# Kernel optimization log

Hardware: AMD Instinct MI355X
Metric: run time of the kernel (lower is better)

The kernel has to match this reference:

```python
import jax, jax.numpy as jnp
import numpy as np

D_MODEL = 1024
HEAD_DIM = D_MODEL // 16  # num_heads=16, used only for the softmax scale
EPS = 1e-5


def _layernorm(x, g, b):
    mu = jnp.mean(x, axis=-1, keepdims=True)
    var = jnp.var(x, axis=-1, keepdims=True)
    return (x - mu) * jax.lax.rsqrt(var + EPS) * g + b


def setup_inputs() -> dict:
    key = jax.random.key(0)
    ks = jax.random.split(key, 16)
    d, dff = D_MODEL, 4 * D_MODEL
    s = 1.0 / np.sqrt(d)
    inp = {
        "x": jax.random.normal(ks[0], (4, 2048, d), dtype=jnp.float32),
        "wq": jax.random.normal(ks[1], (d, d), dtype=jnp.float32) * s,
        "bq": jnp.zeros((d,), jnp.float32),
        "wk": jax.random.normal(ks[2], (d, d), dtype=jnp.float32) * s,
        "bk": jnp.zeros((d,), jnp.float32),
        "wv": jax.random.normal(ks[3], (d, d), dtype=jnp.float32) * s,
        "bv": jnp.zeros((d,), jnp.float32),
        "wo": jax.random.normal(ks[4], (d, d), dtype=jnp.float32) * s,
        "bo": jnp.zeros((d,), jnp.float32),
        "w1": jax.random.normal(ks[5], (d, dff), dtype=jnp.float32) * s,
        "b1": jnp.zeros((dff,), jnp.float32),
        "w2": jax.random.normal(ks[6], (dff, d), dtype=jnp.float32) * (1.0 / np.sqrt(dff)),
        "b2": jnp.zeros((d,), jnp.float32),
        "g1": jnp.ones((d,), jnp.float32),
        "be1": jnp.zeros((d,), jnp.float32),
        "g2": jnp.ones((d,), jnp.float32),
        "be2": jnp.zeros((d,), jnp.float32),
    }
    return inp


def reference(x, wq, bq, wk, bk, wv, bv, wo, bo, w1, b1, w2, b2, g1, be1, g2, be2):
    # --- attention sub-block (NOTE: no head split in original module) ---
    residual = x
    h = _layernorm(x, g1, be1)
    q = h @ wq + bq
    k = h @ wk + bk
    v = h @ wv + bv
    scale = 1.0 / np.sqrt(HEAD_DIM)
    scores = jnp.einsum("bsd,btd->bst", q, k) * scale  # [B,S,S]
    attn = jax.nn.softmax(scores, axis=-1)
    ctx = jnp.einsum("bst,btd->bsd", attn, v)
    x = ctx @ wo + bo + residual
    # --- MLP sub-block ---
    residual = x
    h = _layernorm(x, g2, be2)
    h = jax.nn.gelu(h @ w1 + b1, approximate=False)
    return h @ w2 + b2 + residual
```

## Files before the change

kernel.cpp:

```cpp
#include <hip/hip_runtime.h>
#include <hip/hip_bf16.h>

typedef __hip_bfloat16 bf16;
typedef __attribute__((ext_vector_type(8))) short short8;
typedef __attribute__((ext_vector_type(4))) float floatx4;

__device__ __forceinline__ unsigned short f2bf(float x) {
  unsigned u = __builtin_bit_cast(unsigned, x);
  unsigned r = (u + 0x7fffu + ((u >> 16) & 1u)) >> 16;
  return (unsigned short)r;
}

#define GLL(g, l) __builtin_amdgcn_global_load_lds(                                  \
    (const __attribute__((address_space(1))) void*)(g),                              \
    (__attribute__((address_space(3))) void*)(l), 16, 0, 0)

template <int N> __device__ __forceinline__ void vmwait() {
  asm volatile("s_waitcnt vmcnt(%0)" ::"i"(N) : "memory");
}

__global__ __launch_bounds__(256) void wtrans_kernel(const float* __restrict__ in,
                                                     bf16* __restrict__ out,
                                                     int K, int N) {
  __shared__ float tile[32][33];
  int tx = threadIdx.x, ty = threadIdx.y;
  int n0 = blockIdx.x * 32, k0 = blockIdx.y * 32;
#pragma unroll
  for (int i = 0; i < 32; i += 8)
    tile[ty + i][tx] = in[(size_t)(k0 + ty + i) * N + (n0 + tx)];
  __syncthreads();
#pragma unroll
  for (int i = 0; i < 32; i += 8)
    out[(size_t)(n0 + ty + i) * K + (k0 + tx)] = __float2bfloat16(tile[tx][ty + i]);
}

__global__ __launch_bounds__(256) void ln_kernel(const float* __restrict__ x,
                                                 const float* __restrict__ g,
                                                 const float* __restrict__ b,
                                                 bf16* __restrict__ out) {
  const int D = 1024;
  size_t row = blockIdx.x;
  int t = threadIdx.x;
  float4 v = ((const float4*)(x + row * D))[t];
  float s  = v.x + v.y + v.z + v.w;
  float ss = v.x * v.x + v.y * v.y + v.z * v.z + v.w * v.w;
#pragma unroll
  for (int off = 32; off > 0; off >>= 1) {
    s  += __shfl_xor(s, off);
    ss += __shfl_xor(ss, off);
  }
  __shared__ float rs[4], rss[4];
  int wv = t >> 6;
  if ((t & 63) == 0) { rs[wv] = s; rss[wv] = ss; }
  __syncthreads();
  s  = rs[0] + rs[1] + rs[2] + rs[3];
  ss = rss[0] + rss[1] + rss[2] + rss[3];
  float mu  = s * (1.f / D);
  float inv = rsqrtf(ss * (1.f / D) - mu * mu + 1e-5f);
  float4 gv = ((const float4*)g)[t];
  float4 bv = ((const float4*)b)[t];
  ushort4 o;
  o.x = f2bf((v.x - mu) * inv * gv.x + bv.x);
  o.y = f2bf((v.y - mu) * inv * gv.y + bv.y);
  o.z = f2bf((v.z - mu) * inv * gv.z + bv.z);
  o.w = f2bf((v.w - mu) * inv * gv.w + bv.w);
  ((ushort4*)(out + row * D))[t] = o;
}

__global__ __launch_bounds__(256) void softmax_kernel(float* sc) {
  const int S = 2048;
  float* p = sc + (size_t)blockIdx.x * S;
  int t = threadIdx.x;
  float4 v0 = ((const float4*)p)[2 * t];
  float4 v1 = ((const float4*)p)[2 * t + 1];
  float f[8] = {v0.x, v0.y, v0.z, v0.w, v1.x, v1.y, v1.z, v1.w};
  float m = f[0];
#pragma unroll
  for (int j = 1; j < 8; ++j) m = fmaxf(m, f[j]);
#pragma unroll
  for (int off = 32; off > 0; off >>= 1) m = fmaxf(m, __shfl_xor(m, off));
  __shared__ float r1[4], r2[4];
  int wv = t >> 6;
  if ((t & 63) == 0) r1[wv] = m;
  __syncthreads();
  m = fmaxf(fmaxf(r1[0], r1[1]), fmaxf(r1[2], r1[3]));
  float s = 0.f;
#pragma unroll
  for (int j = 0; j < 8; ++j) { f[j] = __expf(f[j] - m); s += f[j]; }
#pragma unroll
  for (int off = 32; off > 0; off >>= 1) s += __shfl_xor(s, off);
  if ((t & 63) == 0) r2[wv] = s;
  __syncthreads();
  s = r2[0] + r2[1] + r2[2] + r2[3];
  float inv = 1.f / s;
  unsigned u0 = f2bf(f[0] * inv), u1 = f2bf(f[1] * inv);
  unsigned u2 = f2bf(f[2] * inv), u3 = f2bf(f[3] * inv);
  unsigned u4 = f2bf(f[4] * inv), u5 = f2bf(f[5] * inv);
  unsigned u6 = f2bf(f[6] * inv), u7 = f2bf(f[7] * inv);
  uint4 o;
  o.x = u0 | (u1 << 16);
  o.y = u2 | (u3 << 16);
  o.z = u4 | (u5 << 16);
  o.w = u6 | (u7 << 16);
  ((uint4*)p)[t] = o;
}

template <int NF, bool OUT_BF16, bool HAS_BIAS, bool HAS_RES, bool GELU, bool VTR>
__global__ __launch_bounds__(512, 2) void gemm4q(
    const bf16* __restrict__ A, int lda, size_t sA,
    const bf16* __restrict__ BT, int ldb, size_t sB,
    void* Cv, size_t sC,
    const float* __restrict__ bias, const float* res, bf16* vtr,
    int N, int K, float alpha, int gx, int gy) {
  constexpr int BN = NF * 64;
  constexpr int NI = NF / 2;
  constexpr int BHALF = NF == 4 ? 16384 : 8192;
  constexpr int W_A = 4;
  constexpr int W_B = NF == 4 ? 4 : 3;
  __shared__ __align__(16) char lds[65536 + (NF == 4 ? 65536 : 32768)];
  char* const ldsA = lds;
  char* const ldsB = lds + 65536;

  const int tid = threadIdx.x;
  const int lane = tid & 63;
  const int wave = tid >> 6;
  const int wm = wave >> 2, wn = wave & 3;
  const int lr = lane & 15, lq = lane >> 4;

  int id = blockIdx.x;
  const int nwg = gridDim.x;
  if ((nwg & 7) == 0) id = (id & 7) * (nwg >> 3) + (id >> 3);
  const int bx = id % gx;
  const int rem = id / gx;
  const int by = rem % gy;
  const int bz = rem / gy;
  const int m0 = by * 256, n0 = bx * BN;

  const int srow = tid >> 3;
  const int schunk = ((tid & 7) ^ (srow & 7)) * 8;
  const bf16* gA = A + sA * bz + (size_t)(m0 + srow) * lda + schunk;
  const bf16* gB = BT + sB * bz + (size_t)(n0 + srow) * ldb + schunk;

  const int nk = K >> 6;

  auto stA = [&](int tt, int h) {
    if (tt < nk) {
      const bf16* s = gA + (size_t)(h * 128) * lda + (size_t)tt * 64;
      char* d = ldsA + (((tt & 1) * 2 + h) << 14) + tid * 16;
      GLL(s, d);
      GLL(s + (size_t)64 * lda, d + 8192);
    }
  };
  auto stB = [&](int tt, int h) {
    if (tt < nk) {
      const bf16* s = gB + (size_t)(h * (BN / 2)) * ldb + (size_t)tt * 64;
      char* d = ldsB + ((tt & 1) * 2 + h) * BHALF + tid * 16;
      GLL(s, d);
      if constexpr (NF == 4) GLL(s + (size_t)64 * ldb, d + 8192);
    }
  };

  const int aB0 = (wm * 64 + lr) * 128 + ((lq ^ (lr & 7)) << 4);
  const int aB1 = aB0 ^ 64;
  const int bRow = (NF == 4) ? (wn * 32 + lr) : (wn * 16 + lr);
  const int bB0 = bRow * 128 + ((lq ^ (lr & 7)) << 4);
  const int bB1 = bB0 ^ 64;

  floatx4 acc[2][2][4][NI] = {};

  stA(0, 0); stB(0, 0); stB(0, 1); stA(0, 1);
  vmwait<W_B>();
  __builtin_amdgcn_s_barrier();

  for (int t = 0; t < nk; ++t) {
    const char* As0 = ldsA + (((t & 1) * 2 + 0) << 14);
    const char* As1 = ldsA + (((t & 1) * 2 + 1) << 14);
    const char* Bs0 = ldsB + ((t & 1) * 2 + 0) * BHALF;
    const char* Bs1 = ldsB + ((t & 1) * 2 + 1) * BHALF;
    short8 a0[4], a1[4], b0[NI], b1[NI];

#pragma unroll
    for (int mi = 0; mi < 4; ++mi) {
      a0[mi] = *(const short8*)(As0 + aB0 + mi * 2048);
      a1[mi] = *(const short8*)(As0 + aB1 + mi * 2048);
    }
#pragma unroll
    for (int ni = 0; ni < NI; ++ni) {
      b0[ni] = *(const short8*)(Bs0 + bB0 + ni * 2048);
      b1[ni] = *(const short8*)(Bs0 + bB1 + ni * 2048);
    }
    stA(t + 1, 0);
    asm volatile("s_waitcnt lgkmcnt(0)" ::: "memory");
    __builtin_amdgcn_sched_barrier(0);
    __builtin_amdgcn_s_setprio(1);
#pragma unroll
    for (int mi = 0; mi < 4; ++mi)
#pragma unroll
      for (int ni = 0; ni < NI; ++ni)
        acc[0][0][mi][ni] = __builtin_amdgcn_mfma_f32_16x16x32_bf16(a0[mi], b0[ni], acc[0][0][mi][ni], 0, 0, 0);
#pragma unroll
    for (int mi = 0; mi < 4; ++mi)
#pragma unroll
      for (int ni = 0; ni < NI; ++ni)
        acc[0][0][mi][ni] = __builtin_amdgcn_mfma_f32_16x16x32_bf16(a1[mi], b1[ni], acc[0][0][mi][ni], 0, 0, 0);
    __builtin_amdgcn_s_setprio(0);
    vmwait<W_A>();
    __builtin_amdgcn_s_barrier();

#pragma unroll
    for (int ni = 0; ni < NI; ++ni) {
      b0[ni] = *(const short8*)(Bs1 + bB0 + ni * 2048);
      b1[ni] = *(const short8*)(Bs1 + bB1 + ni * 2048);
    }
    stB(t + 1, 0);
    asm volatile("s_waitcnt lgkmcnt(0)" ::: "memory");
    __builtin_amdgcn_sched_barrier(0);
    __builtin_amdgcn_s_setprio(1);
#pragma unroll
    for (int mi = 0; mi < 4; ++mi)
#pragma unroll
      for (int ni = 0; ni < NI; ++ni)
        acc[0][1][mi][ni] = __builtin_amdgcn_mfma_f32_16x16x32_bf16(a0[mi], b0[ni], acc[0][1][mi][ni], 0, 0, 0);
#pragma unroll
    for (int mi = 0; mi < 4; ++mi)
#pragma unroll
      for (int ni = 0; ni < NI; ++ni)
        acc[0][1][mi][ni] = __builtin_amdgcn_mfma_f32_16x16x32_bf16(a1[mi], b1[ni], acc[0][1][mi][ni], 0, 0, 0);
    __builtin_amdgcn_s_setprio(0);
    vmwait<W_B>();
    __builtin_amdgcn_s_barrier();

#pragma unroll
    for (int mi = 0; mi < 4; ++mi) {
      a0[mi] = *(const short8*)(As1 + aB0 + mi * 2048);
      a1[mi] = *(const short8*)(As1 + aB1 + mi * 2048);
    }
    stB(t + 1, 1);
    asm volatile("s_waitcnt lgkmcnt(0)" ::: "memory");
    __builtin_amdgcn_sched_barrier(0);
    __builtin_amdgcn_s_setprio(1);
#pragma unroll
    for (int mi = 0; mi < 4; ++mi)
#pragma unroll
      for (int ni = 0; ni < NI; ++ni)
        acc[1][1][mi][ni] = __builtin_amdgcn_mfma_f32_16x16x32_bf16(a0[mi], b0[ni], acc[1][1][mi][ni], 0, 0, 0);
#pragma unroll
    for (int mi = 0; mi < 4; ++mi)
#pragma unroll
      for (int ni = 0; ni < NI; ++ni)
        acc[1][1][mi][ni] = __builtin_amdgcn_mfma_f32_16x16x32_bf16(a1[mi], b1[ni], acc[1][1][mi][ni], 0, 0, 0);
    __builtin_amdgcn_s_setprio(0);
    __builtin_amdgcn_s_barrier();

#pragma unroll
    for (int ni = 0; ni < NI; ++ni) {
      b0[ni] = *(const short8*)(Bs0 + bB0 + ni * 2048);
      b1[ni] = *(const short8*)(Bs0 + bB1 + ni * 2048);
    }
    stA(t + 1, 1);
    asm volatile("s_waitcnt lgkmcnt(0)" ::: "memory");
    __builtin_amdgcn_sched_barrier(0);
    __builtin_amdgcn_s_setprio(1);
#pragma unroll
    for (int mi = 0; mi < 4; ++mi)
#pragma unroll
      for (int ni = 0; ni < NI; ++ni)
        acc[1][0][mi][ni] = __builtin_amdgcn_mfma_f32_16x16x32_bf16(a0[mi], b0[ni], acc[1][0][mi][ni], 0, 0, 0);
#pragma unroll
    for (int mi = 0; mi < 4; ++mi)
#pragma unroll
      for (int ni = 0; ni < NI; ++ni)
        acc[1][0][mi][ni] = __builtin_amdgcn_mfma_f32_16x16x32_bf16(a1[mi], b1[ni], acc[1][0][mi][ni], 0, 0, 0);
    __builtin_amdgcn_s_setprio(0);
    vmwait<W_B>();
    __builtin_amdgcn_s_barrier();
  }

  float* Cf = (float*)Cv;
  bf16* Cb = (bf16*)Cv;
  const size_t cb = sC * bz;
#pragma unroll
  for (int mq = 0; mq < 2; ++mq)
#pragma unroll
    for (int nq = 0; nq < 2; ++nq)
#pragma unroll
      for (int mi = 0; mi < 4; ++mi) {
        const int row = m0 + mq * 128 + wm * 64 + mi * 16 + lq * 4;
#pragma unroll
        for (int ni = 0; ni < NI; ++ni) {
          const int col = n0 + nq * (BN / 2) + wn * (BN / 8) + ni * 16 + lr;
          const float bb = HAS_BIAS ? bias[col] : 0.f;
#pragma unroll
          for (int r = 0; r < 4; ++r) {
            float val = acc[mq][nq][mi][ni][r] * alpha + bb;
            if (GELU) val = 0.5f * val * (1.f + erff(val * 0.70710678118654752f));
            if (HAS_RES) val += res[(size_t)(row + r) * N + col];
            const size_t idx = cb + (size_t)(row + r) * N + col;
            if (OUT_BF16) Cb[idx] = __float2bfloat16(val);
            else Cf[idx] = val;
            if (VTR) {
              if (col >= 2048) {
                const int rr = row + r;
                vtr[(((size_t)(rr >> 11) << 10) + (col - 2048)) * 2048 + (rr & 2047)] =
                    __float2bfloat16(val);
              }
            }
          }
        }
      }
}

extern "C" void kernel_launch(void* const* d_in, const int* in_sizes, int n_in,
                              void* d_out, int out_size, void* d_ws, size_t ws_size,
                              hipStream_t stream) {
  const int B = 4, S = 2048, D = 1024, DFF = 4096;
  const int M = B * S;
  const float* x   = (const float*)d_in[0];
  const float* wq  = (const float*)d_in[1];
  const float* bq  = (const float*)d_in[2];
  const float* wk  = (const float*)d_in[3];
  const float* bk  = (const float*)d_in[4];
  const float* wv  = (const float*)d_in[5];
  const float* bv  = (const float*)d_in[6];
  const float* wo  = (const float*)d_in[7];
  const float* bo  = (const float*)d_in[8];
  const float* w1  = (const float*)d_in[9];
  const float* b1  = (const float*)d_in[10];
  const float* w2  = (const float*)d_in[11];
  const float* b2  = (const float*)d_in[12];
  const float* g1  = (const float*)d_in[13];
  const float* be1 = (const float*)d_in[14];
  const float* g2  = (const float*)d_in[15];
  const float* be2 = (const float*)d_in[16];
  float* out = (float*)d_out;

  char* wsb = (char*)d_ws;
  const size_t MB1 = 1ull << 20;
  bf16* wqkvT = (bf16*)(wsb + 0 * MB1);
  bf16* woT   = (bf16*)(wsb + 6 * MB1);
  bf16* w1T   = (bf16*)(wsb + 8 * MB1);
  bf16* w2T   = (bf16*)(wsb + 16 * MB1);
  float* bqkv = (float*)(wsb + 24 * MB1);
  bf16* h     = (bf16*)(wsb + 25 * MB1);
  bf16* qkv   = (bf16*)(wsb + 41 * MB1);
  bf16* hidden = (bf16*)(wsb + 41 * MB1);
  bf16* vTall = (bf16*)(wsb + 89 * MB1);
  float* sc   = (float*)(wsb + 105 * MB1);

  int chunk = 1;
  if (ws_size > 105 * MB1) {
    size_t c = (ws_size - 105 * MB1) / (16 * MB1);
    chunk = (int)(c > 4 ? 4 : (c < 1 ? 1 : c));
  }

  dim3 tb(32, 8);
  wtrans_kernel<<<dim3(32, 32), tb, 0, stream>>>(wq, wqkvT, D, D);
  wtrans_kernel<<<dim3(32, 32), tb, 0, stream>>>(wk, wqkvT + (size_t)1024 * 1024, D, D);
  wtrans_kernel<<<dim3(32, 32), tb, 0, stream>>>(wv, wqkvT + (size_t)2048 * 1024, D, D);
  wtrans_kernel<<<dim3(32, 32), tb, 0, stream>>>(wo, woT, D, D);
  wtrans_kernel<<<dim3(128, 32), tb, 0, stream>>>(w1, w1T, D, DFF);
  wtrans_kernel<<<dim3(32, 128), tb, 0, stream>>>(w2, w2T, DFF, D);
  hipMemcpyAsync(bqkv, bq, 4096, hipMemcpyDeviceToDevice, stream);
  hipMemcpyAsync(bqkv + 1024, bk, 4096, hipMemcpyDeviceToDevice, stream);
  hipMemcpyAsync(bqkv + 2048, bv, 4096, hipMemcpyDeviceToDevice, stream);

  ln_kernel<<<M, 256, 0, stream>>>(x, g1, be1, h);

  gemm4q<2, true, true, false, false, true><<<24 * 32, 512, 0, stream>>>(
      h, D, 0, wqkvT, D, 0, qkv, 0, bqkv, nullptr, vTall, 3072, D, 1.f, 24, 32);

  for (int b0 = 0; b0 < B; b0 += chunk) {
    int c = (B - b0 < chunk) ? (B - b0) : chunk;
    gemm4q<4, false, false, false, false, false><<<64 * c, 512, 0, stream>>>(
        qkv + (size_t)b0 * S * 3072, 3072, (size_t)S * 3072,
        qkv + (size_t)b0 * S * 3072 + 1024, 3072, (size_t)S * 3072,
        sc, (size_t)S * S, nullptr, nullptr, nullptr, S, D, 0.125f, 8, 8);
    softmax_kernel<<<c * S, 256, 0, stream>>>(sc);
    gemm4q<2, true, false, false, false, false><<<64 * c, 512, 0, stream>>>(
        (const bf16*)sc, 2 * S, (size_t)S * 2 * S,
        vTall + (size_t)b0 * D * S, S, (size_t)D * S,
        h + (size_t)b0 * S * D, (size_t)S * D, nullptr, nullptr, nullptr, D, S, 1.f, 8, 8);
  }

  gemm4q<2, false, true, true, false, false><<<8 * 32, 512, 0, stream>>>(
      h, D, 0, woT, D, 0, out, 0, bo, x, nullptr, D, D, 1.f, 8, 32);

  ln_kernel<<<M, 256, 0, stream>>>(out, g2, be2, h);

  gemm4q<4, true, true, false, true, false><<<16 * 32, 512, 0, stream>>>(
      h, D, 0, w1T, D, 0, hidden, 0, b1, nullptr, nullptr, DFF, D, 1.f, 16, 32);

  gemm4q<2, false, true, true, false, false><<<8 * 32, 512, 0, stream>>>(
      hidden, DFF, 0, w2T, DFF, 0, out, 0, b2, out, nullptr, D, DFF, 1.f, 8, 32);
}
```

Measured before the change: 473.4 us.

## Rewrite GEMM pipeline with deeper prefetch, wave-major tiles, and inline-asm LDS reads

Replaces the gemm4q template with two specialized kernels. gemm9w handles 256x256 tiles and gemm9n handles 256x128 tiles. Both prefetch two k-steps ahead with a staggered per-quadrant load schedule, issue LDS reads through inline ds_read_b128 with immediate offsets, and peel the final iterations to drain vmcnt correctly. Each wave now owns a contiguous 128-row block rather than interleaved halves, and the QKV projection moves to the wide 256-column tile with half as many workgroups. The goal is to hide global-load latency and cut address arithmetic and barrier stalls. The cost is more barriers per step, heavier register pressure, and fewer workgroups for the QKV GEMM.

```diff
diff --git a/kernel.cpp b/kernel.cpp
--- a/kernel.cpp
+++ b/kernel.cpp
@@ -4,6 +4,9 @@
 typedef __hip_bfloat16 bf16;
 typedef __attribute__((ext_vector_type(8))) short short8;
 typedef __attribute__((ext_vector_type(4))) float floatx4;
+typedef __attribute__((address_space(3))) char c3;
+
+template <int V> struct ic { static constexpr int value = V; };
 
 __device__ __forceinline__ unsigned short f2bf(float x) {
   unsigned u = __builtin_bit_cast(unsigned, x);
@@ -18,6 +21,16 @@
 template <int N> __device__ __forceinline__ void vmwait() {
   asm volatile("s_waitcnt vmcnt(%0)" ::"i"(N) : "memory");
 }
+template <int N> __device__ __forceinline__ void lgkwait() {
+  asm volatile("s_waitcnt lgkmcnt(%0)" ::"i"(N) : "memory");
+  __builtin_amdgcn_sched_barrier(0);
+}
+template <int OFF> __device__ __forceinline__ short8 dsr(unsigned a) {
+  short8 r;
+  asm volatile("ds_read_b128 %0, %1 offset:%2" : "=v"(r) : "v"(a), "i"(OFF));
+  return r;
+}
+#define MFMA_(d, a, b) d = __builtin_amdgcn_mfma_f32_16x16x32_bf16(a, b, d, 0, 0, 0)
 
 __global__ __launch_bounds__(256) void wtrans_kernel(const float* __restrict__ in,
                                                      bf16* __restrict__ out,
@@ -105,21 +118,15 @@
   ((uint4*)p)[t] = o;
 }
 
-template <int NF, bool OUT_BF16, bool HAS_BIAS, bool HAS_RES, bool GELU, bool VTR>
-__global__ __launch_bounds__(512, 2) void gemm4q(
+template <bool OUT_BF16, bool HAS_BIAS, bool HAS_RES, bool GELU, bool VTR>
+__global__ __launch_bounds__(512, 2) void gemm9w(
     const bf16* __restrict__ A, int lda, size_t sA,
     const bf16* __restrict__ BT, int ldb, size_t sB,
     void* Cv, size_t sC,
     const float* __restrict__ bias, const float* res, bf16* vtr,
     int N, int K, float alpha, int gx, int gy) {
-  constexpr int BN = NF * 64;
-  constexpr int NI = NF / 2;
-  constexpr int BHALF = NF == 4 ? 16384 : 8192;
-  constexpr int W_A = 4;
-  constexpr int W_B = NF == 4 ? 4 : 3;
-  __shared__ __align__(16) char lds[65536 + (NF == 4 ? 65536 : 32768)];
-  char* const ldsA = lds;
-  char* const ldsB = lds + 65536;
+  __shared__ __align__(16) char ldsb[131072];
+  const unsigned lds0 = (unsigned)(uintptr_t)(c3*)ldsb;
 
   const int tid = threadIdx.x;
   const int lane = tid & 63;
@@ -134,165 +141,153 @@
   const int rem = id / gx;
   const int by = rem % gy;
   const int bz = rem / gy;
-  const int m0 = by * 256, n0 = bx * BN;
-
-  const int srow = tid >> 3;
-  const int schunk = ((tid & 7) ^ (srow & 7)) * 8;
-  const bf16* gA = A + sA * bz + (size_t)(m0 + srow) * lda + schunk;
-  const bf16* gB = BT + sB * bz + (size_t)(n0 + srow) * ldb + schunk;
+  const int m0 = by * 256, n0 = bx * 256;
+
+  const int sidx = tid >> 3;
+  const int schunk = ((tid & 7) ^ (sidx & 7)) * 8;
+  const bf16* gA = A + sA * bz + (size_t)(m0 + sidx) * lda + schunk;
+  const int rowB = ((sidx >> 5) << 6) + (sidx & 31);
+  const bf16* gB = BT + sB * bz + (size_t)(n0 + rowB) * ldb + schunk;
 
   const int nk = K >> 6;
 
   auto stA = [&](int tt, int h) {
     if (tt < nk) {
-      const bf16* s = gA + (size_t)(h * 128) * lda + (size_t)tt * 64;
-      char* d = ldsA + (((tt & 1) * 2 + h) << 14) + tid * 16;
+      const bf16* s = gA + (size_t)(h * 64) * lda + (size_t)tt * 64;
+      char* d = ldsb + (((tt & 1) * 2 + h) << 14) + tid * 16;
       GLL(s, d);
-      GLL(s + (size_t)64 * lda, d + 8192);
+      GLL(s + (size_t)128 * lda, d + 8192);
     }
   };
-  auto stB = [&](int tt, int h) {
+  auto stB = [&](int tt, int g) {
     if (tt < nk) {
-      const bf16* s = gB + (size_t)(h * (BN / 2)) * ldb + (size_t)tt * 64;
-      char* d = ldsB + ((tt & 1) * 2 + h) * BHALF + tid * 16;
+      const bf16* s = gB + (size_t)(g * 32) * ldb + (size_t)tt * 64;
+      char* d = ldsb + 65536 + (((tt & 1) * 2 + g) << 14) + tid * 16;
       GLL(s, d);
-      if constexpr (NF == 4) GLL(s + (size_t)64 * ldb, d + 8192);
+      GLL(s + (size_t)128 * ldb, d + 8192);
     }
   };
 
-  const int aB0 = (wm * 64 + lr) * 128 + ((lq ^ (lr & 7)) << 4);
-  const int aB1 = aB0 ^ 64;
-  const int bRow = (NF == 4) ? (wn * 32 + lr) : (wn * 16 + lr);
-  const int bB0 = bRow * 128 + ((lq ^ (lr & 7)) << 4);
-  const int bB1 = bB0 ^ 64;
-
-  floatx4 acc[2][2][4][NI] = {};
+  const unsigned aoff = (wm * 64 + lr) * 128 + ((lq ^ (lr & 7)) << 4);
+  const unsigned boff = (wn * 32 + lr) * 128 + ((lq ^ (lr & 7)) << 4);
+
+  floatx4 acc[2][2][4][2] = {};
 
   stA(0, 0); stB(0, 0); stB(0, 1); stA(0, 1);
-  vmwait<W_B>();
+  stA(1, 0); stB(1, 0); stB(1, 1);
+  vmwait<6>();
   __builtin_amdgcn_s_barrier();
 
-  for (int t = 0; t < nk; ++t) {
-    const char* As0 = ldsA + (((t & 1) * 2 + 0) << 14);
-    const char* As1 = ldsA + (((t & 1) * 2 + 1) << 14);
-    const char* Bs0 = ldsB + ((t & 1) * 2 + 0) * BHALF;
-    const char* Bs1 = ldsB + ((t & 1) * 2 + 1) * BHALF;
-    short8 a0[4], a1[4], b0[NI], b1[NI];
-
-#pragma unroll
-    for (int mi = 0; mi < 4; ++mi) {
-      a0[mi] = *(const short8*)(As0 + aB0 + mi * 2048);
-      a1[mi] = *(const short8*)(As0 + aB1 + mi * 2048);
-    }
-#pragma unroll
-    for (int ni = 0; ni < NI; ++ni) {
-      b0[ni] = *(const short8*)(Bs0 + bB0 + ni * 2048);
-      b1[ni] = *(const short8*)(Bs0 + bB1 + ni * 2048);
-    }
-    stA(t + 1, 0);
-    asm volatile("s_waitcnt lgkmcnt(0)" ::: "memory");
-    __builtin_amdgcn_sched_barrier(0);
+  auto body = [&](int kt, auto modeC) {
+    constexpr int MODE = decltype(modeC)::value;
+    const unsigned p = (unsigned)(kt & 1);
+    const unsigned Aa = lds0 + ((p * 2 + 0) << 14);
+    const unsigned Ab = lds0 + ((p * 2 + 1) << 14);
+    const unsigned Bg = lds0 + 65536 + ((p * 2 + 0) << 14);
+    const unsigned Bd = lds0 + 65536 + ((p * 2 + 1) << 14);
+    short8 a0[4], a1[4], g0[2], g1[2], d0[2], d1[2];
+
+    {
+      const unsigned aA = Aa + aoff, aX = aA ^ 64;
+      a0[0] = dsr<0>(aA); a0[1] = dsr<2048>(aA); a0[2] = dsr<4096>(aA); a0[3] = dsr<6144>(aA);
+      a1[0] = dsr<0>(aX); a1[1] = dsr<2048>(aX); a1[2] = dsr<4096>(aX); a1[3] = dsr<6144>(aX);
+      const unsigned bA = Bg + boff, bX = bA ^ 64;
+      g0[0] = dsr<0>(bA); g0[1] = dsr<2048>(bA);
+      g1[0] = dsr<0>(bX); g1[1] = dsr<2048>(bX);
+    }
+    stA(kt + 1, 1);
+    __builtin_amdgcn_s_barrier();
+    lgkwait<0>();
     __builtin_amdgcn_s_setprio(1);
 #pragma unroll
     for (int mi = 0; mi < 4; ++mi)
 #pragma unroll
-      for (int ni = 0; ni < NI; ++ni)
-        acc[0][0][mi][ni] = __builtin_amdgcn_mfma_f32_16x16x32_bf16(a0[mi], b0[ni], acc[0][0][mi][ni], 0, 0, 0);
-#pragma unroll
-    for (int mi = 0; mi < 4; ++mi)
-#pragma unroll
-      for (int ni = 0; ni < NI; ++ni)
-        acc[0][0][mi][ni] = __builtin_amdgcn_mfma_f32_16x16x32_bf16(a1[mi], b1[ni], acc[0][0][mi][ni], 0, 0, 0);
+      for (int nl = 0; nl < 2; ++nl) MFMA_(acc[0][0][mi][nl], a0[mi], g0[nl]);
+#pragma unroll
+    for (int mi = 0; mi < 4; ++mi)
+#pragma unroll
+      for (int nl = 0; nl < 2; ++nl) MFMA_(acc[0][0][mi][nl], a1[mi], g1[nl]);
     __builtin_amdgcn_s_setprio(0);
-    vmwait<W_A>();
-    __builtin_amdgcn_s_barrier();
-
-#pragma unroll
-    for (int ni = 0; ni < NI; ++ni) {
-      b0[ni] = *(const short8*)(Bs1 + bB0 + ni * 2048);
-      b1[ni] = *(const short8*)(Bs1 + bB1 + ni * 2048);
-    }
-    stB(t + 1, 0);
-    asm volatile("s_waitcnt lgkmcnt(0)" ::: "memory");
-    __builtin_amdgcn_sched_barrier(0);
+    __builtin_amdgcn_s_barrier();
+
+    {
+      const unsigned bA = Bd + boff, bX = bA ^ 64;
+      d0[0] = dsr<0>(bA); d0[1] = dsr<2048>(bA);
+      d1[0] = dsr<0>(bX); d1[1] = dsr<2048>(bX);
+    }
+    stA(kt + 2, 0);
+    __builtin_amdgcn_s_barrier();
+    lgkwait<0>();
     __builtin_amdgcn_s_setprio(1);
 #pragma unroll
     for (int mi = 0; mi < 4; ++mi)
 #pragma unroll
-      for (int ni = 0; ni < NI; ++ni)
-        acc[0][1][mi][ni] = __builtin_amdgcn_mfma_f32_16x16x32_bf16(a0[mi], b0[ni], acc[0][1][mi][ni], 0, 0, 0);
-#pragma unroll
-    for (int mi = 0; mi < 4; ++mi)
-#pragma unroll
-      for (int ni = 0; ni < NI; ++ni)
-        acc[0][1][mi][ni] = __builtin_amdgcn_mfma_f32_16x16x32_bf16(a1[mi], b1[ni], acc[0][1][mi][ni], 0, 0, 0);
+      for (int nl = 0; nl < 2; ++nl) MFMA_(acc[0][1][mi][nl], a0[mi], d0[nl]);
+#pragma unroll
+    for (int mi = 0; mi < 4; ++mi)
+#pragma unroll
+      for (int nl = 0; nl < 2; ++nl) MFMA_(acc[0][1][mi][nl], a1[mi], d1[nl]);
     __builtin_amdgcn_s_setprio(0);
-    vmwait<W_B>();
-    __builtin_amdgcn_s_barrier();
-
-#pragma unroll
-    for (int mi = 0; mi < 4; ++mi) {
-      a0[mi] = *(const short8*)(As1 + aB0 + mi * 2048);
-      a1[mi] = *(const short8*)(As1 + aB1 + mi * 2048);
-    }
-    stB(t + 1, 1);
-    asm volatile("s_waitcnt lgkmcnt(0)" ::: "memory");
-    __builtin_amdgcn_sched_barrier(0);
+    __builtin_amdgcn_s_barrier();
+
+    {
+      const unsigned aA = Ab + aoff, aX = aA ^ 64;
+      a0[0] = dsr<0>(aA); a0[1] = dsr<2048>(aA); a0[2] = dsr<4096>(aA); a0[3] = dsr<6144>(aA);
+      a1[0] = dsr<0>(aX); a1[1] = dsr<2048>(aX); a1[2] = dsr<4096>(aX); a1[3] = dsr<6144>(aX);
+    }
+    stB(kt + 2, 0);
+    __builtin_amdgcn_s_barrier();
+    lgkwait<0>();
     __builtin_amdgcn_s_setprio(1);
 #pragma unroll
     for (int mi = 0; mi < 4; ++mi)
 #pragma unroll
-      for (int ni = 0; ni < NI; ++ni)
-        acc[1][1][mi][ni] = __builtin_amdgcn_mfma_f32_16x16x32_bf16(a0[mi], b0[ni], acc[1][1][mi][ni], 0, 0, 0);
-#pragma unroll
-    for (int mi = 0; mi < 4; ++mi)
-#pragma unroll
-      for (int ni = 0; ni < NI; ++ni)
-        acc[1][1][mi][ni] = __builtin_amdgcn_mfma_f32_16x16x32_bf16(a1[mi], b1[ni], acc[1][1][mi][ni], 0, 0, 0);
+      for (int nl = 0; nl < 2; ++nl) MFMA_(acc[1][1][mi][nl], a0[mi], d0[nl]);
+#pragma unroll
+    for (int mi = 0; mi < 4; ++mi)
+#pragma unroll
+      for (int nl = 0; nl < 2; ++nl) MFMA_(acc[1][1][mi][nl], a1[mi], d1[nl]);
     __builtin_amdgcn_s_setprio(0);
     __builtin_amdgcn_s_barrier();
 
-#pragma unroll
-    for (int ni = 0; ni < NI; ++ni) {
-      b0[ni] = *(const short8*)(Bs0 + bB0 + ni * 2048);
-      b1[ni] = *(const short8*)(Bs0 + bB1 + ni * 2048);
-    }
-    stA(t + 1, 1);
-    asm volatile("s_waitcnt lgkmcnt(0)" ::: "memory");
-    __builtin_amdgcn_sched_barrier(0);
+    stB(kt + 2, 1);
+    __builtin_amdgcn_s_barrier();
     __builtin_amdgcn_s_setprio(1);
 #pragma unroll
     for (int mi = 0; mi < 4; ++mi)
 #pragma unroll
-      for (int ni = 0; ni < NI; ++ni)
-        acc[1][0][mi][ni] = __builtin_amdgcn_mfma_f32_16x16x32_bf16(a0[mi], b0[ni], acc[1][0][mi][ni], 0, 0, 0);
-#pragma unroll
-    for (int mi = 0; mi < 4; ++mi)
-#pragma unroll
-      for (int ni = 0; ni < NI; ++ni)
-        acc[1][0][mi][ni] = __builtin_amdgcn_mfma_f32_16x16x32_bf16(a1[mi], b1[ni], acc[1][0][mi][ni], 0, 0, 0);
+      for (int nl = 0; nl < 2; ++nl) MFMA_(acc[1][0][mi][nl], a0[mi], g0[nl]);
+#pragma unroll
+    for (int mi = 0; mi < 4; ++mi)
+#pragma unroll
+      for (int nl = 0; nl < 2; ++nl) MFMA_(acc[1][0][mi][nl], a1[mi], g1[nl]);
     __builtin_amdgcn_s_setprio(0);
-    vmwait<W_B>();
-    __builtin_amdgcn_s_barrier();
-  }
+    if constexpr (MODE == 0) vmwait<6>();
+    else if constexpr (MODE == 1) vmwait<0>();
+    __builtin_amdgcn_s_barrier();
+  };
+
+  for (int kt = 0; kt + 2 < nk; ++kt) body(kt, ic<0>{});
+  body(nk - 2, ic<1>{});
+  body(nk - 1, ic<2>{});
 
   float* Cf = (float*)Cv;
   bf16* Cb = (bf16*)Cv;
   const size_t cb = sC * bz;
 #pragma unroll
-  for (int mq = 0; mq < 2; ++mq)
-#pragma unroll
-    for (int nq = 0; nq < 2; ++nq)
+  for (int mh = 0; mh < 2; ++mh)
+#pragma unroll
+    for (int ng = 0; ng < 2; ++ng)
 #pragma unroll
       for (int mi = 0; mi < 4; ++mi) {
-        const int row = m0 + mq * 128 + wm * 64 + mi * 16 + lq * 4;
-#pragma unroll
-        for (int ni = 0; ni < NI; ++ni) {
-          const int col = n0 + nq * (BN / 2) + wn * (BN / 8) + ni * 16 + lr;
+        const int row = m0 + wm * 128 + (mh * 4 + mi) * 16 + lq * 4;
+#pragma unroll
+        for (int nl = 0; nl < 2; ++nl) {
+          const int col = n0 + wn * 64 + (ng * 2 + nl) * 16 + lr;
           const float bb = HAS_BIAS ? bias[col] : 0.f;
 #pragma unroll
           for (int r = 0; r < 4; ++r) {
-            float val = acc[mq][nq][mi][ni][r] * alpha + bb;
+            float val = acc[mh][ng][mi][nl][r] * alpha + bb;
             if (GELU) val = 0.5f * val * (1.f + erff(val * 0.70710678118654752f));
             if (HAS_RES) val += res[(size_t)(row + r) * N + col];
             const size_t idx = cb + (size_t)(row + r) * N + col;
@@ -308,6 +303,155 @@
           }
         }
       }
+}
+
+template <bool OUT_BF16, bool HAS_BIAS, bool HAS_RES, bool GELU, bool VTR>
+__global__ __launch_bounds__(512, 2) void gemm9n(
+    const bf16* __restrict__ A, int lda, size_t sA,
+    const bf16* __restrict__ BT, int ldb, size_t sB,
+    void* Cv, size_t sC,
+    const float* __restrict__ bias, const float* res, bf16* vtr,
+    int N, int K, float alpha, int gx, int gy) {
+  __shared__ __align__(16) char ldsb[98304];
+  const unsigned lds0 = (unsigned)(uintptr_t)(c3*)ldsb;
+
+  const int tid = threadIdx.x;
+  const int lane = tid & 63;
+  const int wave = tid >> 6;
+  const int wm = wave >> 2, wn = wave & 3;
+  const int lr = lane & 15, lq = lane >> 4;
+
+  int id = blockIdx.x;
+  const int nwg = gridDim.x;
+  if ((nwg & 7) == 0) id = (id & 7) * (nwg >> 3) + (id >> 3);
+  const int bx = id % gx;
+  const int rem = id / gx;
+  const int by = rem % gy;
+  const int bz = rem / gy;
+  const int m0 = by * 256, n0 = bx * 128;
+
+  const int sidx = tid >> 3;
+  const int schunk = ((tid & 7) ^ (sidx & 7)) * 8;
+  const bf16* gA = A + sA * bz + (size_t)(m0 + sidx) * lda + schunk;
+  const bf16* gB = BT + sB * bz + (size_t)(n0 + sidx) * ldb + schunk;
+
+  const int nk = K >> 6;
+
+  auto stA = [&](int tt, int h) {
+    if (tt < nk) {
+      const bf16* s = gA + (size_t)(h * 64) * lda + (size_t)tt * 64;
+      char* d = ldsb + (((tt & 1) * 2 + h) << 14) + tid * 16;
+      GLL(s, d);
+      GLL(s + (size_t)128 * lda, d + 8192);
+    }
+  };
+  auto stBn = [&](int tt) {
+    if (tt < nk) {
+      const bf16* s = gB + (size_t)tt * 64;
+      char* d = ldsb + 65536 + ((tt & 1) << 14) + tid * 16;
+      GLL(s, d);
+      GLL(s + (size_t)64 * ldb, d + 8192);
+    }
+  };
+
+  const unsigned aoff = (wm * 64 + lr) * 128 + ((lq ^ (lr & 7)) << 4);
+  const unsigned boff = (wn * 32 + lr) * 128 + ((lq ^ (lr & 7)) << 4);
+
+  floatx4 acc[2][4][2] = {};
+
+  stA(0, 0); stBn(0); stA(0, 1);
+  stA(1, 0); stBn(1);
+  vmwait<4>();
+  __builtin_amdgcn_s_barrier();
+
+  auto body = [&](int kt, auto modeC) {
+    constexpr int MODE = decltype(modeC)::value;
+    const unsigned p = (unsigned)(kt & 1);
+    const unsigned Aa = lds0 + ((p * 2 + 0) << 14);
+    const unsigned Ab = lds0 + ((p * 2 + 1) << 14);
+    const unsigned Bb = lds0 + 65536 + (p << 14);
+    short8 a0[4], a1[4], b0[2], b1[2];
+
+    {
+      const unsigned aA = Aa + aoff, aX = aA ^ 64;
+      a0[0] = dsr<0>(aA); a0[1] = dsr<2048>(aA); a0[2] = dsr<4096>(aA); a0[3] = dsr<6144>(aA);
+      a1[0] = dsr<0>(aX); a1[1] = dsr<2048>(aX); a1[2] = dsr<4096>(aX); a1[3] = dsr<6144>(aX);
+      const unsigned bA = Bb + boff, bX = bA ^ 64;
+      b0[0] = dsr<0>(bA); b0[1] = dsr<2048>(bA);
+      b1[0] = dsr<0>(bX); b1[1] = dsr<2048>(bX);
+    }
+    stA(kt + 1, 1);
+    __builtin_amdgcn_s_barrier();
+    lgkwait<0>();
+    __builtin_amdgcn_s_setprio(1);
+#pragma unroll
+    for (int mi = 0; mi < 4; ++mi)
+#pragma unroll
+      for (int nl = 0; nl < 2; ++nl) MFMA_(acc[0][mi][nl], a0[mi], b0[nl]);
+#pragma unroll
+    for (int mi = 0; mi < 4; ++mi)
+#pragma unroll
+      for (int nl = 0; nl < 2; ++nl) MFMA_(acc[0][mi][nl], a1[mi], b1[nl]);
+    __builtin_amdgcn_s_setprio(0);
+    __builtin_amdgcn_s_barrier();
+
+    {
+      const unsigned aA = Ab + aoff, aX = aA ^ 64;
+      a0[0] = dsr<0>(aA); a0[1] = dsr<2048>(aA); a0[2] = dsr<4096>(aA); a0[3] = dsr<6144>(aA);
+      a1[0] = dsr<0>(aX); a1[1] = dsr<2048>(aX); a1[2] = dsr<4096>(aX); a1[3] = dsr<6144>(aX);
+    }
+    stA(kt + 2, 0); stBn(kt + 2);
+    __builtin_amdgcn_s_barrier();
+    lgkwait<0>();
+    __builtin_amdgcn_s_setprio(1);
+#pragma unroll
+    for (int mi = 0; mi < 4; ++mi)
+#pragma unroll
+      for (int nl = 0; nl < 2; ++nl) MFMA_(acc[1][mi][nl], a0[mi], b0[nl]);
+#pragma unroll
+    for (int mi = 0; mi < 4; ++mi)
+#pragma unroll
+      for (int nl = 0; nl < 2; ++nl) MFMA_(acc[1][mi][nl], a1[mi], b1[nl]);
+    __builtin_amdgcn_s_setprio(0);
+    if constexpr (MODE == 0) vmwait<4>();
+    else if constexpr (MODE == 1) vmwait<0>();
+    __builtin_amdgcn_s_barrier();
+  };
+
+  for (int kt = 0; kt + 2 < nk; ++kt) body(kt, ic<0>{});
+  body(nk - 2, ic<1>{});
+  body(nk - 1, ic<2>{});
+
+  float* Cf = (float*)Cv;
+  bf16* Cb = (bf16*)Cv;
+  const size_t cb = sC * bz;
+#pragma unroll
+  for (int mh = 0; mh < 2; ++mh)
+#pragma unroll
+    for (int mi = 0; mi < 4; ++mi) {
+      const int row = m0 + wm * 128 + (mh * 4 + mi) * 16 + lq * 4;
+#pragma unroll
+      for (int nl = 0; nl < 2; ++nl) {
+        const int col = n0 + wn * 32 + nl * 16 + lr;
+        const float bb = HAS_BIAS ? bias[col] : 0.f;
+#pragma unroll
+        for (int r = 0; r < 4; ++r) {
+          float val = acc[mh][mi][nl][r] * alpha + bb;
+          if (GELU) val = 0.5f * val * (1.f + erff(val * 0.70710678118654752f));
+          if (HAS_RES) val += res[(size_t)(row + r) * N + col];
+          const size_t idx = cb + (size_t)(row + r) * N + col;
+          if (OUT_BF16) Cb[idx] = __float2bfloat16(val);
+          else Cf[idx] = val;
+          if (VTR) {
+            if (col >= 2048) {
+              const int rr = row + r;
+              vtr[(((size_t)(rr >> 11) << 10) + (col - 2048)) * 2048 + (rr & 2047)] =
+                  __float2bfloat16(val);
+            }
+          }
+        }
+      }
+    }
 }
 
 extern "C" void kernel_launch(void* const* d_in, const int* in_sizes, int n_in,
@@ -366,30 +510,30 @@
 
   ln_kernel<<<M, 256, 0, stream>>>(x, g1, be1, h);
 
-  gemm4q<2, true, true, false, false, true><<<24 * 32, 512, 0, stream>>>(
-      h, D, 0, wqkvT, D, 0, qkv, 0, bqkv, nullptr, vTall, 3072, D, 1.f, 24, 32);
+  gemm9w<true, true, false, false, true><<<12 * 32, 512, 0, stream>>>(
+      h, D, 0, wqkvT, D, 0, qkv, 0, bqkv, nullptr, vTall, 3072, D, 1.f, 12, 32);
 
   for (int b0 = 0; b0 < B; b0 += chunk) {
     int c = (B - b0 < chunk) ? (B - b0) : chunk;
-    gemm4q<4, false, false, false, false, false><<<64 * c, 512, 0, stream>>>(
+    gemm9w<false, false, false, false, false><<<64 * c, 512, 0, stream>>>(
         qkv + (size_t)b0 * S * 3072, 3072, (size_t)S * 3072,
         qkv + (size_t)b0 * S * 3072 + 1024, 3072, (size_t)S * 3072,
         sc, (size_t)S * S, nullptr, nullptr, nullptr, S, D, 0.125f, 8, 8);
     softmax_kernel<<<c * S, 256, 0, stream>>>(sc);
-    gemm4q<2, true, false, false, false, false><<<64 * c, 512, 0, stream>>>(
+    gemm9n<true, false, false, false, false><<<64 * c, 512, 0, stream>>>(
         (const bf16*)sc, 2 * S, (size_t)S * 2 * S,
         vTall + (size_t)b0 * D * S, S, (size_t)D * S,
         h + (size_t)b0 * S * D, (size_t)S * D, nullptr, nullptr, nullptr, D, S, 1.f, 8, 8);
   }
 
-  gemm4q<2, false, true, true, false, false><<<8 * 32, 512, 0, stream>>>(
+  gemm9n<false, true, true, false, false><<<8 * 32, 512, 0, stream>>>(
       h, D, 0, woT, D, 0, out, 0, bo, x, nullptr, D, D, 1.f, 8, 32);
 
   ln_kernel<<<M, 256, 0, stream>>>(out, g2, be2, h);
 
-  gemm4q<4, true, true, false, true, false><<<16 * 32, 512, 0, stream>>>(
+  gemm9w<true, true, false, true, false><<<16 * 32, 512, 0, stream>>>(
       h, D, 0, w1T, D, 0, hidden, 0, b1, nullptr, nullptr, DFF, D, 1.f, 16, 32);
 
-  gemm4q<2, false, true, true, false, false><<<8 * 32, 512, 0, stream>>>(
+  gemm9n<false, true, true, false, false><<<8 * 32, 512, 0, stream>>>(
       hidden, DFF, 0, w2T, DFF, 0, out, 0, b2, out, nullptr, D, DFF, 1.f, 8, 32);
 }
```

Result: no change. 469.6 us (-0.8%).
